# Performance work log

Measured on AMD Instinct MI355X. Metric: run time of the kernel, lower is better.

Reference implementation:

```python
import jax, jax.numpy as jnp
import numpy as np

D_MODEL = 1024
N_HEADS = 16
HEAD_DIM = D_MODEL // N_HEADS


def setup_inputs() -> dict:
    key = jax.random.key(0)
    ks = jax.random.split(key, 9)
    s = 1.0 / np.sqrt(D_MODEL)
    inp = {"x": jax.random.normal(ks[0], (4, 2048, D_MODEL), dtype=jnp.float32)}
    for i, name in enumerate(["q", "k", "v", "o"]):
        inp[f"W{name}"] = jax.random.uniform(ks[1 + i], (D_MODEL, D_MODEL), dtype=jnp.float32, minval=-s, maxval=s)
        inp[f"b{name}"] = jax.random.uniform(ks[5 + i], (D_MODEL,), dtype=jnp.float32, minval=-s, maxval=s)
    return inp


def reference(x, Wq, Wk, Wv, Wo, bq, bk, bv, bo):
    B, S, D = x.shape
    # linear layers: y = x @ W^T + b (torch nn.Linear convention)
    def proj(W, b):
        y = jnp.einsum('bsd,ed->bse', x, W) + b
        return y.reshape(B, S, N_HEADS, HEAD_DIM).transpose(0, 2, 1, 3)  # [B,H,S,hd]
    q = proj(Wq, bq)
    k = proj(Wk, bk)
    v = proj(Wv, bv)
    score = jnp.einsum('bhqd,bhkd->bhqk', q, k) / np.sqrt(HEAD_DIM)  # [B,H,S,S]
    attns = jax.nn.softmax(score, axis=-1)
    out = jnp.einsum('bhqk,bhkd->bhqd', attns, v)  # [B,H,S,hd]
    out = out.transpose(0, 2, 1, 3).reshape(B, S, D)
    return jnp.einsum('bsd,ed->bse', out, Wo) + bo
```

## Files before the change

### kernel.cpp

```cpp
#include <hip/hip_runtime.h>
#include <hip/hip_bf16.h>
#include <stdint.h>


typedef __attribute__((ext_vector_type(8))) short bfx8;
typedef __attribute__((ext_vector_type(4))) float fx4;

#define MFMA_16x16x32(A, B, C) __builtin_amdgcn_mfma_f32_16x16x32_bf16(A, B, C, 0, 0, 0)

__device__ __forceinline__ unsigned short f2bf(float f) {
  union { float f; uint32_t u; } v; v.f = f;
  uint32_t r = v.u + 0x7fffu + ((v.u >> 16) & 1u);
  return (unsigned short)(r >> 16);
}
__device__ __forceinline__ unsigned short bf16u(float f) {
  union { __hip_bfloat16 h; unsigned short u; } cv;
  cv.h = __float2bfloat16(f);
  return cv.u;
}
__device__ __forceinline__ void async16(unsigned short* l, const unsigned short* g) {
  __builtin_amdgcn_global_load_lds((const __attribute__((address_space(1))) void*)g,
                                   (__attribute__((address_space(3))) void*)l,
                                   16, 0, 0);
}

__global__ __launch_bounds__(256) void convert_f32_bf16(
    const float* __restrict__ src, unsigned short* __restrict__ dst, int n4) {
  const int i = blockIdx.x * 256 + threadIdx.x;
  if (i >= n4) return;
  const float4 v = ((const float4*)src)[i];
  ushort4 o;
  o.x = f2bf(v.x); o.y = f2bf(v.y); o.z = f2bf(v.z); o.w = f2bf(v.w);
  ((ushort4*)dst)[i] = o;
}

__global__ __launch_bounds__(256) void convert3_f32_bf16(
    const float* __restrict__ s0, const float* __restrict__ s1,
    const float* __restrict__ s2,
    unsigned short* __restrict__ d0, unsigned short* __restrict__ d1,
    unsigned short* __restrict__ d2, int n4) {
  const int which = blockIdx.y;
  const float* src = (which == 0) ? s0 : ((which == 1) ? s1 : s2);
  unsigned short* dst = (which == 0) ? d0 : ((which == 1) ? d1 : d2);
  const int i = blockIdx.x * 256 + threadIdx.x;
  if (i >= n4) return;
  const float4 v = ((const float4*)src)[i];
  ushort4 o;
  o.x = f2bf(v.x); o.y = f2bf(v.y); o.z = f2bf(v.z); o.w = f2bf(v.w);
  ((ushort4*)dst)[i] = o;
}


__global__ __launch_bounds__(256) void gemm_qkv(
    const unsigned short* __restrict__ X,
    const unsigned short* __restrict__ Wq, const unsigned short* __restrict__ Wk,
    const unsigned short* __restrict__ Wv,
    const float* __restrict__ bq, const float* __restrict__ bk,
    const float* __restrict__ bv,
    unsigned short* __restrict__ outq, unsigned short* __restrict__ outk,
    unsigned short* __restrict__ outv) {
  __shared__ unsigned short ldsA[2][128 * 32];
  __shared__ unsigned short ldsB[2][128 * 32];
  const int tid = threadIdx.x;
  const int w = tid >> 6, lane = tid & 63, quad = lane >> 4, l15 = lane & 15;
  const int m0 = blockIdx.x * 128;
  const int which = blockIdx.y >> 3;
  const int n0 = (blockIdx.y & 7) * 128;
  const unsigned short* W = (which == 0) ? Wq : ((which == 1) ? Wk : Wv);
  const float* bias       = (which == 0) ? bq : ((which == 1) ? bk : bv);
  unsigned short* Y       = (which == 0) ? outq : ((which == 1) ? outk : outv);
  const int wm = (w >> 1) * 64, wn = (w & 1) * 64;
  const int srow = tid >> 2, sseg = tid & 3;
  const int sx = (srow >> 1) & 3;
  const int swcol = ((sseg ^ sx) * 8);
  const int sdst = srow * 32 + sseg * 8;
  const unsigned short* Xa = X + (size_t)(m0 + srow) * 1024 + swcol;
  const unsigned short* Xb = X + (size_t)(m0 + srow + 64) * 1024 + swcol;
  const unsigned short* Wa = W + (size_t)(n0 + srow) * 1024 + swcol;
  const unsigned short* Wb = W + (size_t)(n0 + srow + 64) * 1024 + swcol;
  const int xr = (l15 >> 1) & 3;
  const int rseg = (quad ^ xr) * 8;
  fx4 acc[4][4] = {};

  auto stage = [&](int buf, int k0) {
    async16(&ldsA[buf][sdst],            Xa + k0);
    async16(&ldsA[buf][sdst + 64 * 32],  Xb + k0);
    async16(&ldsB[buf][sdst],            Wa + k0);
    async16(&ldsB[buf][sdst + 64 * 32],  Wb + k0);
  };
  auto compute = [&](int buf) {
    bfx8 af[4], bfr[4];
#pragma unroll
    for (int i = 0; i < 4; i++) af[i]  = *(const bfx8*)&ldsA[buf][(wm + i * 16 + l15) * 32 + rseg];
#pragma unroll
    for (int j = 0; j < 4; j++) bfr[j] = *(const bfx8*)&ldsB[buf][(wn + j * 16 + l15) * 32 + rseg];
#pragma unroll
    for (int i = 0; i < 4; i++)
#pragma unroll
      for (int j = 0; j < 4; j++)
        acc[i][j] = MFMA_16x16x32(af[i], bfr[j], acc[i][j]);
  };

  stage(0, 0);
  __syncthreads();
  int cur = 0;
  for (int t = 0; t < 31; ++t) {
    stage(cur ^ 1, (t + 1) * 32);
    compute(cur);
    __syncthreads();
    cur ^= 1;
  }
  compute(cur);

  const float qscale = 0.18033688011112042f;
  float bv_[4];
#pragma unroll
  for (int j = 0; j < 4; j++) bv_[j] = bias[n0 + wn + j * 16 + l15];
  if (which == 2) {
#pragma unroll
    for (int i = 0; i < 4; i++) {
      const int m_g = m0 + wm + i * 16 + quad * 4;
      const int bb = m_g >> 11, ss = m_g & 2047;
#pragma unroll
      for (int j = 0; j < 4; j++) {
        const int n_g = n0 + wn + j * 16 + l15;
        const int h = n_g >> 6, d = n_g & 63;
        ushort4 o4;
        o4.x = f2bf(acc[i][j][0] + bv_[j]);
        o4.y = f2bf(acc[i][j][1] + bv_[j]);
        o4.z = f2bf(acc[i][j][2] + bv_[j]);
        o4.w = f2bf(acc[i][j][3] + bv_[j]);
        *(ushort4*)&Y[((size_t)(bb * 16 + h) * 64 + d) * 2048 + ss] = o4;
      }
    }
  } else {
#pragma unroll
    for (int i = 0; i < 4; i++) {
#pragma unroll
      for (int r = 0; r < 4; r++) {
        const int m_g = m0 + wm + i * 16 + quad * 4 + r;
        const int bb = m_g >> 11, ss = m_g & 2047;
#pragma unroll
        for (int j = 0; j < 4; j++) {
          const int n_g = n0 + wn + j * 16 + l15;
          const int h = n_g >> 6, d = n_g & 63;
          float o = acc[i][j][r] + bv_[j];
          if (which == 0) o *= qscale;
          Y[(((size_t)(bb * 16 + h)) * 2048 + ss) * 64 + d] = f2bf(o);
        }
      }
    }
  }
}

__global__ __launch_bounds__(256) void gemm_o(
    const unsigned short* __restrict__ X,
    const unsigned short* __restrict__ W,
    const float* __restrict__ bias,
    float* __restrict__ Y) {
  __shared__ unsigned short ldsA[2][128 * 32];
  __shared__ unsigned short ldsB[2][128 * 32];
  const int tid = threadIdx.x;
  const int w = tid >> 6, lane = tid & 63, quad = lane >> 4, l15 = lane & 15;
  const int m0 = blockIdx.x * 128;
  const int n0 = blockIdx.y * 128;
  const int wm = (w >> 1) * 64, wn = (w & 1) * 64;
  const int srow = tid >> 2, sseg = tid & 3;
  const int sx = (srow >> 1) & 3;
  const int swcol = ((sseg ^ sx) * 8);
  const int sdst = srow * 32 + sseg * 8;
  const unsigned short* Xa = X + (size_t)(m0 + srow) * 1024 + swcol;
  const unsigned short* Xb = X + (size_t)(m0 + srow + 64) * 1024 + swcol;
  const unsigned short* Wa = W + (size_t)(n0 + srow) * 1024 + swcol;
  const unsigned short* Wb = W + (size_t)(n0 + srow + 64) * 1024 + swcol;
  const int xr = (l15 >> 1) & 3;
  const int rseg = (quad ^ xr) * 8;
  fx4 acc[4][4] = {};

  auto stage = [&](int buf, int k0) {
    async16(&ldsA[buf][sdst],            Xa + k0);
    async16(&ldsA[buf][sdst + 64 * 32],  Xb + k0);
    async16(&ldsB[buf][sdst],            Wa + k0);
    async16(&ldsB[buf][sdst + 64 * 32],  Wb + k0);
  };
  auto compute = [&](int buf) {
    bfx8 af[4], bfr[4];
#pragma unroll
    for (int i = 0; i < 4; i++) af[i]  = *(const bfx8*)&ldsA[buf][(wm + i * 16 + l15) * 32 + rseg];
#pragma unroll
    for (int j = 0; j < 4; j++) bfr[j] = *(const bfx8*)&ldsB[buf][(wn + j * 16 + l15) * 32 + rseg];
#pragma unroll
    for (int i = 0; i < 4; i++)
#pragma unroll
      for (int j = 0; j < 4; j++)
        acc[i][j] = MFMA_16x16x32(af[i], bfr[j], acc[i][j]);
  };

  stage(0, 0);
  __syncthreads();
  int cur = 0;
  for (int t = 0; t < 31; ++t) {
    stage(cur ^ 1, (t + 1) * 32);
    compute(cur);
    __syncthreads();
    cur ^= 1;
  }
  compute(cur);

  float bv_[4];
#pragma unroll
  for (int j = 0; j < 4; j++) bv_[j] = bias[n0 + wn + j * 16 + l15];
#pragma unroll
  for (int i = 0; i < 4; i++) {
#pragma unroll
    for (int r = 0; r < 4; r++) {
      const int m_g = m0 + wm + i * 16 + quad * 4 + r;
#pragma unroll
      for (int j = 0; j < 4; j++) {
        const int n_g = n0 + wn + j * 16 + l15;
        Y[(size_t)m_g * 1024 + n_g] = acc[i][j][r] + bv_[j];
      }
    }
  }
}


#define P_LD 68

__global__ __launch_bounds__(256, 4) void attn_kernel(
    const unsigned short* __restrict__ Q, const unsigned short* __restrict__ K,
    const unsigned short* __restrict__ VT, unsigned short* __restrict__ O,
    int base) {
  __shared__ unsigned short lds_k[64 * 64];
  __shared__ unsigned short lds_vt[64 * 64];
  __shared__ unsigned short lds_p[4][32 * P_LD];
  const int tid = threadIdx.x;
  const int w = tid >> 6, lane = tid & 63, quad = lane >> 4, l15 = lane & 15;

  const int lin = blockIdx.x;
  const int xcd = lin & 7;
  const int jj = (lin >> 3) + base * 64;
  const int bh = ((jj >> 4) << 3) | xcd;
  const int qb = jj & 15;

  const size_t hoff = (size_t)bh * 2048 * 64;
  const unsigned short* Qh = Q + hoff;
  const unsigned short* Kh = K + hoff;
  const unsigned short* VTh = VT + hoff;
  const int q0 = qb * 128 + w * 32;

  bfx8 qf[2][2];
#pragma unroll
  for (int s = 0; s < 2; s++) {
    qf[s][0] = *(const bfx8*)&Qh[(size_t)(q0 + s * 16 + l15) * 64 + quad * 8];
    qf[s][1] = *(const bfx8*)&Qh[(size_t)(q0 + s * 16 + l15) * 64 + 32 + quad * 8];
  }

  fx4 o_acc[2][4] = {};
  float l_r[2][4] = {};

  const int vr0 = w * 8 + (lane >> 3);
  const int vr1 = vr0 + 32;
  const int seg = lane & 7;
  const unsigned short* vsrc0 = VTh + (size_t)vr0 * 2048 + ((seg ^ (vr0 & 7)) * 8);
  const unsigned short* vsrc1 = VTh + (size_t)vr1 * 2048 + ((seg ^ (vr1 & 7)) * 8);
  unsigned short* vdst0 = &lds_vt[vr0 * 64 + seg * 8];
  unsigned short* vdst1 = &lds_vt[vr1 * 64 + seg * 8];

  const int krl = lane >> 3;
  unsigned short* kdst0 = &lds_k[(w * 16 + krl) * 64 + seg * 8];
  unsigned short* kdst1 = kdst0 + 8 * 64;
  const unsigned short* ksrc0 = Kh + (size_t)(w * 16 + krl) * 64 + ((seg ^ krl) * 8);
  const unsigned short* ksrc1 = ksrc0 + 8 * 64;

  const int s0v = (quad ^ (l15 & 7)) * 8;
  const int s1v = ((quad + 4) ^ (l15 & 7)) * 8;

  async16(kdst0, ksrc0);
  async16(kdst1, ksrc1);

  for (int t = 0; t < 32; ++t) {
    const int kv0 = t * 64;
    __syncthreads();
    async16(vdst0, vsrc0 + kv0);
    async16(vdst1, vsrc1 + kv0);

    fx4 s0a[4], s1a[4];
#pragma unroll
    for (int nj = 0; nj < 4; nj++) {
      const int krow = (nj * 16 + l15) * 64;
      bfx8 kf0 = *(const bfx8*)&lds_k[krow + s0v];
      bfx8 kf1 = *(const bfx8*)&lds_k[krow + s1v];
      fx4 z0 = {}, z1 = {};
      z0 = MFMA_16x16x32(qf[0][0], kf0, z0);
      z0 = MFMA_16x16x32(qf[0][1], kf1, z0);
      z1 = MFMA_16x16x32(qf[1][0], kf0, z1);
      z1 = MFMA_16x16x32(qf[1][1], kf1, z1);
      s0a[nj] = z0;
      s1a[nj] = z1;
    }

#pragma unroll
    for (int s = 0; s < 2; s++) {
      const fx4* sa = (s == 0) ? s0a : s1a;
#pragma unroll
      for (int r = 0; r < 4; r++) {
        float p0 = __builtin_amdgcn_exp2f(sa[0][r]);
        float p1 = __builtin_amdgcn_exp2f(sa[1][r]);
        float p2 = __builtin_amdgcn_exp2f(sa[2][r]);
        float p3 = __builtin_amdgcn_exp2f(sa[3][r]);
        l_r[s][r] += (p0 + p1) + (p2 + p3);
        const int pbase = (s * 16 + quad * 4 + r) * P_LD + l15;
        lds_p[w][pbase]      = bf16u(p0);
        lds_p[w][pbase + 16] = bf16u(p1);
        lds_p[w][pbase + 32] = bf16u(p2);
        lds_p[w][pbase + 48] = bf16u(p3);
      }
    }

    __syncthreads();

    bfx8 pf[2][2];
#pragma unroll
    for (int s = 0; s < 2; s++) {
      pf[s][0] = *(const bfx8*)&lds_p[w][(s * 16 + l15) * P_LD + quad * 8];
      pf[s][1] = *(const bfx8*)&lds_p[w][(s * 16 + l15) * P_LD + 32 + quad * 8];
    }
#pragma unroll
    for (int nj = 0; nj < 4; nj++) {
      const int vrow = (nj * 16 + l15) * 64;
      bfx8 vf0 = *(const bfx8*)&lds_vt[vrow + s0v];
      bfx8 vf1 = *(const bfx8*)&lds_vt[vrow + s1v];
      o_acc[0][nj] = MFMA_16x16x32(pf[0][0], vf0, o_acc[0][nj]);
      o_acc[0][nj] = MFMA_16x16x32(pf[0][1], vf1, o_acc[0][nj]);
      o_acc[1][nj] = MFMA_16x16x32(pf[1][0], vf0, o_acc[1][nj]);
      o_acc[1][nj] = MFMA_16x16x32(pf[1][1], vf1, o_acc[1][nj]);
    }

    if (t < 31) {
      const size_t koff = (size_t)(t + 1) * 64 * 64;
      async16(kdst0, ksrc0 + koff);
      async16(kdst1, ksrc1 + koff);
    }
  }

  const int bb = bh >> 4, h = bh & 15;
#pragma unroll
  for (int s = 0; s < 2; s++) {
#pragma unroll
    for (int r = 0; r < 4; r++) {
      float sum = l_r[s][r];
#pragma unroll
      for (int d = 1; d < 16; d <<= 1) sum += __shfl_xor(sum, d, 64);
      const float inv = 1.0f / sum;
      const int qrow = q0 + s * 16 + quad * 4 + r;
      const size_t base2 = ((size_t)(bb * 2048 + qrow)) * 1024 + h * 64;
#pragma unroll
      for (int nj = 0; nj < 4; nj++)
        O[base2 + nj * 16 + l15] = f2bf(o_acc[s][nj][r] * inv);
    }
  }
}


extern "C" void kernel_launch(void* const* d_in, const int* in_sizes, int n_in,
                              void* d_out, int out_size, void* d_ws, size_t ws_size,
                              hipStream_t stream) {
  const float* x = (const float*)d_in[0];
  const float *Wq, *Wk, *Wv, *Wo, *bq, *bk, *bv, *bo;
  if (in_sizes[2] == 1024) {
    Wq = (const float*)d_in[1]; bq = (const float*)d_in[2];
    Wk = (const float*)d_in[3]; bk = (const float*)d_in[4];
    Wv = (const float*)d_in[5]; bv = (const float*)d_in[6];
    Wo = (const float*)d_in[7]; bo = (const float*)d_in[8];
  } else {
    Wq = (const float*)d_in[1]; Wk = (const float*)d_in[2];
    Wv = (const float*)d_in[3]; Wo = (const float*)d_in[4];
    bq = (const float*)d_in[5]; bk = (const float*)d_in[6];
    bv = (const float*)d_in[7]; bo = (const float*)d_in[8];
  }
  const size_t NT = (size_t)4 * 16 * 2048 * 64;
  const size_t NW = (size_t)1024 * 1024;
  unsigned short* ws = (unsigned short*)d_ws;
  unsigned short* xb = ws;
  unsigned short* q  = ws + NT;
  unsigned short* k  = ws + 2 * NT;
  unsigned short* vt = ws + 3 * NT;
  unsigned short* ao = xb;
  unsigned short* wq = (unsigned short*)d_out;
  unsigned short* wk = wq + NW;
  unsigned short* wv = wk + NW;
  unsigned short* wo = q;

  convert_f32_bf16<<<(int)(NT / 4 + 255) / 256, 256, 0, stream>>>(x, xb, (int)(NT / 4));
  convert3_f32_bf16<<<dim3((int)(NW / 4 + 255) / 256, 3), 256, 0, stream>>>(
      Wq, Wk, Wv, wq, wk, wv, (int)(NW / 4));

  gemm_qkv<<<dim3(64, 24), 256, 0, stream>>>(xb, wq, wk, wv, bq, bk, bv, q, k, vt);
  attn_kernel<<<dim3(1024), 256, 0, stream>>>(q, k, vt, ao, 0);

  convert_f32_bf16<<<(int)(NW / 4 + 255) / 256, 256, 0, stream>>>(Wo, wo, (int)(NW / 4));
  gemm_o<<<dim3(64, 8), 256, 0, stream>>>(ao, wo, bo, (float*)d_out);
}
```

Baseline: 294.7 us.

## Triple-buffer GEMM LDS stages with partial vmcnt waits to deepen prefetch

Both projection GEMMs (QKV and output) move from double-buffered to triple-buffered LDS staging. Loads are issued two k-steps ahead, and the loop waits with s_waitcnt vmcnt(4), so only the older stage must have landed before the barrier. The aim is to hide global-to-LDS load latency behind the MFMA compute instead of draining all loads every iteration. It raises LDS use per block from 32KB to 48KB, which may lower occupancy, and it relies on hand-placed wait counts being correct.

```diff
diff --git a/kernel.cpp b/kernel.cpp
--- a/kernel.cpp
+++ b/kernel.cpp
@@ -7,6 +7,10 @@
 typedef __attribute__((ext_vector_type(4))) float fx4;
 
 #define MFMA_16x16x32(A, B, C) __builtin_amdgcn_mfma_f32_16x16x32_bf16(A, B, C, 0, 0, 0)
+
+#define VMCNT4 asm volatile("s_waitcnt vmcnt(4)" ::: "memory")
+#define VMCNT0 asm volatile("s_waitcnt vmcnt(0)" ::: "memory")
+#define CFENCE asm volatile("" ::: "memory")
 
 __device__ __forceinline__ unsigned short f2bf(float f) {
   union { float f; uint32_t u; } v; v.f = f;
@@ -59,8 +63,8 @@
     const float* __restrict__ bv,
     unsigned short* __restrict__ outq, unsigned short* __restrict__ outk,
     unsigned short* __restrict__ outv) {
-  __shared__ unsigned short ldsA[2][128 * 32];
-  __shared__ unsigned short ldsB[2][128 * 32];
+  __shared__ unsigned short ldsA[3][128 * 32];
+  __shared__ unsigned short ldsB[3][128 * 32];
   const int tid = threadIdx.x;
   const int w = tid >> 6, lane = tid & 63, quad = lane >> 4, l15 = lane & 15;
   const int m0 = blockIdx.x * 128;
@@ -102,15 +106,19 @@
   };
 
   stage(0, 0);
-  __syncthreads();
-  int cur = 0;
-  for (int t = 0; t < 31; ++t) {
-    stage(cur ^ 1, (t + 1) * 32);
-    compute(cur);
-    __syncthreads();
-    cur ^= 1;
-  }
-  compute(cur);
+  stage(1, 32);
+  VMCNT4;
+  __builtin_amdgcn_s_barrier();
+  CFENCE;
+  for (int t = 0; t < 32; ++t) {
+    if (t < 30) stage((t + 2) % 3, (t + 2) * 32);
+    compute(t % 3);
+    if (t < 31) {
+      if (t < 30) { VMCNT4; } else { VMCNT0; }
+      __builtin_amdgcn_s_barrier();
+      CFENCE;
+    }
+  }
 
   const float qscale = 0.18033688011112042f;
   float bv_[4];
@@ -158,8 +166,8 @@
     const unsigned short* __restrict__ W,
     const float* __restrict__ bias,
     float* __restrict__ Y) {
-  __shared__ unsigned short ldsA[2][128 * 32];
-  __shared__ unsigned short ldsB[2][128 * 32];
+  __shared__ unsigned short ldsA[3][128 * 32];
+  __shared__ unsigned short ldsB[3][128 * 32];
   const int tid = threadIdx.x;
   const int w = tid >> 6, lane = tid & 63, quad = lane >> 4, l15 = lane & 15;
   const int m0 = blockIdx.x * 128;
@@ -197,15 +205,19 @@
   };
 
   stage(0, 0);
-  __syncthreads();
-  int cur = 0;
-  for (int t = 0; t < 31; ++t) {
-    stage(cur ^ 1, (t + 1) * 32);
-    compute(cur);
-    __syncthreads();
-    cur ^= 1;
-  }
-  compute(cur);
+  stage(1, 32);
+  VMCNT4;
+  __builtin_amdgcn_s_barrier();
+  CFENCE;
+  for (int t = 0; t < 32; ++t) {
+    if (t < 30) stage((t + 2) % 3, (t + 2) * 32);
+    compute(t % 3);
+    if (t < 31) {
+      if (t < 30) { VMCNT4; } else { VMCNT0; }
+      __builtin_amdgcn_s_barrier();
+      CFENCE;
+    }
+  }
 
   float bv_[4];
 #pragma unroll
```

Measured after the change: 298.2 us. About the same (+1.2%).

## Double-buffer K/V tiles and widen attention blocks to eight waves

Applied to the files above, without the earlier changes.

The attention kernel now runs 512-thread blocks that each cover 256 query rows, so every K/V tile staged in LDS is shared by eight waves instead of four. K and V^T tiles are double-buffered, with the next tile's async loads issued at the start of each iteration. The second barrier per iteration is removed, relying on the P scratch being private to each wave. LDS per block roughly doubles, and the grid halves, which may reduce scheduling flexibility and latency hiding.

```diff
diff --git a/kernel.cpp b/kernel.cpp
--- a/kernel.cpp
+++ b/kernel.cpp
@@ -227,27 +227,26 @@
 
 #define P_LD 68
 
-__global__ __launch_bounds__(256, 4) void attn_kernel(
+__global__ __launch_bounds__(512, 4) void attn_kernel(
     const unsigned short* __restrict__ Q, const unsigned short* __restrict__ K,
-    const unsigned short* __restrict__ VT, unsigned short* __restrict__ O,
-    int base) {
-  __shared__ unsigned short lds_k[64 * 64];
-  __shared__ unsigned short lds_vt[64 * 64];
-  __shared__ unsigned short lds_p[4][32 * P_LD];
+    const unsigned short* __restrict__ VT, unsigned short* __restrict__ O) {
+  __shared__ unsigned short lds_k[2][64 * 64];
+  __shared__ unsigned short lds_vt[2][64 * 64];
+  __shared__ unsigned short lds_p[8][32 * P_LD];
   const int tid = threadIdx.x;
   const int w = tid >> 6, lane = tid & 63, quad = lane >> 4, l15 = lane & 15;
 
   const int lin = blockIdx.x;
   const int xcd = lin & 7;
-  const int jj = (lin >> 3) + base * 64;
-  const int bh = ((jj >> 4) << 3) | xcd;
-  const int qb = jj & 15;
+  const int jj = lin >> 3;
+  const int bh = ((jj >> 3) << 3) | xcd;
+  const int qb = jj & 7;
 
   const size_t hoff = (size_t)bh * 2048 * 64;
   const unsigned short* Qh = Q + hoff;
   const unsigned short* Kh = K + hoff;
   const unsigned short* VTh = VT + hoff;
-  const int q0 = qb * 128 + w * 32;
+  const int q0 = qb * 256 + w * 32;
 
   bfx8 qf[2][2];
 #pragma unroll
@@ -259,38 +258,33 @@
   fx4 o_acc[2][4] = {};
   float l_r[2][4] = {};
 
-  const int vr0 = w * 8 + (lane >> 3);
-  const int vr1 = vr0 + 32;
-  const int seg = lane & 7;
-  const unsigned short* vsrc0 = VTh + (size_t)vr0 * 2048 + ((seg ^ (vr0 & 7)) * 8);
-  const unsigned short* vsrc1 = VTh + (size_t)vr1 * 2048 + ((seg ^ (vr1 & 7)) * 8);
-  unsigned short* vdst0 = &lds_vt[vr0 * 64 + seg * 8];
-  unsigned short* vdst1 = &lds_vt[vr1 * 64 + seg * 8];
-
-  const int krl = lane >> 3;
-  unsigned short* kdst0 = &lds_k[(w * 16 + krl) * 64 + seg * 8];
-  unsigned short* kdst1 = kdst0 + 8 * 64;
-  const unsigned short* ksrc0 = Kh + (size_t)(w * 16 + krl) * 64 + ((seg ^ krl) * 8);
-  const unsigned short* ksrc1 = ksrc0 + 8 * 64;
+  const int srow = tid >> 3;
+  const int sseg = tid & 7;
+  const int ssw = (sseg ^ (srow & 7)) * 8;
+  const unsigned short* ksrc = Kh + (size_t)srow * 64 + ssw;
+  const unsigned short* vsrc = VTh + (size_t)srow * 2048 + ssw;
+  const int sdst = srow * 64 + sseg * 8;
 
   const int s0v = (quad ^ (l15 & 7)) * 8;
   const int s1v = ((quad + 4) ^ (l15 & 7)) * 8;
 
-  async16(kdst0, ksrc0);
-  async16(kdst1, ksrc1);
-
+  async16(&lds_k[0][sdst], ksrc);
+  async16(&lds_vt[0][sdst], vsrc);
+
+  int buf = 0;
   for (int t = 0; t < 32; ++t) {
-    const int kv0 = t * 64;
     __syncthreads();
-    async16(vdst0, vsrc0 + kv0);
-    async16(vdst1, vsrc1 + kv0);
+    if (t < 31) {
+      async16(&lds_k[buf ^ 1][sdst], ksrc + (size_t)(t + 1) * 64 * 64);
+      async16(&lds_vt[buf ^ 1][sdst], vsrc + (size_t)(t + 1) * 64);
+    }
 
     fx4 s0a[4], s1a[4];
 #pragma unroll
     for (int nj = 0; nj < 4; nj++) {
       const int krow = (nj * 16 + l15) * 64;
-      bfx8 kf0 = *(const bfx8*)&lds_k[krow + s0v];
-      bfx8 kf1 = *(const bfx8*)&lds_k[krow + s1v];
+      bfx8 kf0 = *(const bfx8*)&lds_k[buf][krow + s0v];
+      bfx8 kf1 = *(const bfx8*)&lds_k[buf][krow + s1v];
       fx4 z0 = {}, z1 = {};
       z0 = MFMA_16x16x32(qf[0][0], kf0, z0);
       z0 = MFMA_16x16x32(qf[0][1], kf1, z0);
@@ -318,8 +312,6 @@
       }
     }
 
-    __syncthreads();
-
     bfx8 pf[2][2];
 #pragma unroll
     for (int s = 0; s < 2; s++) {
@@ -329,19 +321,15 @@
 #pragma unroll
     for (int nj = 0; nj < 4; nj++) {
       const int vrow = (nj * 16 + l15) * 64;
-      bfx8 vf0 = *(const bfx8*)&lds_vt[vrow + s0v];
-      bfx8 vf1 = *(const bfx8*)&lds_vt[vrow + s1v];
+      bfx8 vf0 = *(const bfx8*)&lds_vt[buf][vrow + s0v];
+      bfx8 vf1 = *(const bfx8*)&lds_vt[buf][vrow + s1v];
       o_acc[0][nj] = MFMA_16x16x32(pf[0][0], vf0, o_acc[0][nj]);
       o_acc[0][nj] = MFMA_16x16x32(pf[0][1], vf1, o_acc[0][nj]);
       o_acc[1][nj] = MFMA_16x16x32(pf[1][0], vf0, o_acc[1][nj]);
       o_acc[1][nj] = MFMA_16x16x32(pf[1][1], vf1, o_acc[1][nj]);
     }
 
-    if (t < 31) {
-      const size_t koff = (size_t)(t + 1) * 64 * 64;
-      async16(kdst0, ksrc0 + koff);
-      async16(kdst1, ksrc1 + koff);
-    }
+    buf ^= 1;
   }
 
   const int bb = bh >> 4, h = bh & 15;
@@ -397,7 +385,7 @@
       Wq, Wk, Wv, wq, wk, wv, (int)(NW / 4));
 
   gemm_qkv<<<dim3(64, 24), 256, 0, stream>>>(xb, wq, wk, wv, bq, bk, bv, q, k, vt);
-  attn_kernel<<<dim3(1024), 256, 0, stream>>>(q, k, vt, ao, 0);
+  attn_kernel<<<dim3(512), 512, 0, stream>>>(q, k, vt, ao);
 
   convert_f32_bf16<<<(int)(NW / 4 + 255) / 256, 256, 0, stream>>>(Wo, wo, (int)(NW / 4));
   gemm_o<<<dim3(64, 8), 256, 0, stream>>>(ao, wo, bo, (float*)d_out);
```

After: 293.3 us. Within noise of the previous version (-0.5%).
